# Kernel optimization log

Hardware: AMD Instinct MI355X
Metric: run time of the kernel (lower is better)

Reference implementation:

```python
import jax, jax.numpy as jnp
import numpy as np

D, W, H = 128, 128, 128          # volume obj_shape (d, w, h)
RES_SCALE = 1.4
RES_D = int(D * RES_SCALE)       # 179 detector rows
RES_H = int(H * RES_SCALE)       # 179 detector cols
N_PROJ = 10


def setup_inputs() -> dict:
    key = jax.random.key(0)
    k1, k2 = jax.random.split(key, 2)
    # learnable reconstruction volume, initialized to ones (torch.ones_like)
    I_rec = jnp.ones((1, 1, D, W, H), dtype=jnp.float32)
    # emitter positions, scaled to volume size; y-component kept away from the
    # source plane y=0 so that ray directions are well-conditioned
    poses = jax.random.uniform(k1, (50, 3), dtype=jnp.float32)
    poses = poses * jnp.array([D, W, H], jnp.float32) + jnp.array([-64.0, 256.0, -64.0], jnp.float32)
    idx = jax.random.randint(k2, (N_PROJ,), 0, 50, dtype=jnp.int32)
    return {"I_rec": I_rec, "poses": poses, "idx": idx}


def _trilinear_3d(vol, coords):
    """torch F.grid_sample 3D, bilinear, align_corners=False, zero padding.
    vol: [D, Hd, Wd]; coords: [..., 3] in (x, y, z) normalized to [-1, 1],
    where x indexes the last (Wd) axis, y the middle, z the first."""
    Dv, Hv, Wv = vol.shape
    x, y, z = coords[..., 0], coords[..., 1], coords[..., 2]
    ix = ((x + 1.0) * Wv - 1.0) * 0.5
    iy = ((y + 1.0) * Hv - 1.0) * 0.5
    iz = ((z + 1.0) * Dv - 1.0) * 0.5
    x0f, y0f, z0f = jnp.floor(ix), jnp.floor(iy), jnp.floor(iz)
    tx, ty, tz = ix - x0f, iy - y0f, iz - z0f
    x0 = x0f.astype(jnp.int32); y0 = y0f.astype(jnp.int32); z0 = z0f.astype(jnp.int32)
    x1, y1, z1 = x0 + 1, y0 + 1, z0 + 1

    def gather(zc, yc, xc):
        valid = (zc >= 0) & (zc < Dv) & (yc >= 0) & (yc < Hv) & (xc >= 0) & (xc < Wv)
        v = vol[jnp.clip(zc, 0, Dv - 1), jnp.clip(yc, 0, Hv - 1), jnp.clip(xc, 0, Wv - 1)]
        return jnp.where(valid, v, 0.0)

    out = (
        gather(z0, y0, x0) * (1 - tz) * (1 - ty) * (1 - tx)
        + gather(z0, y0, x1) * (1 - tz) * (1 - ty) * tx
        + gather(z0, y1, x0) * (1 - tz) * ty * (1 - tx)
        + gather(z0, y1, x1) * (1 - tz) * ty * tx
        + gather(z1, y0, x0) * tz * (1 - ty) * (1 - tx)
        + gather(z1, y0, x1) * tz * (1 - ty) * tx
        + gather(z1, y1, x0) * tz * ty * (1 - tx)
        + gather(z1, y1, x1) * tz * ty * tx
    )
    return out


def _project_one(vol, emi):
    """vol: [D, W, H]; emi: [3] emitter position. Returns [RES_D, RES_H]."""
    lin_x = jnp.linspace(-RES_D / 2.0, RES_D / 2.0 - 1.0, RES_D, dtype=jnp.float32)
    lin_y = jnp.linspace(-RES_H / 2.0, RES_H / 2.0 - 1.0, RES_H, dtype=jnp.float32)
    gx, gy = jnp.meshgrid(lin_x, lin_y, indexing="ij")            # [Gx, Gy]
    rays = jnp.stack([gx, jnp.zeros_like(gx), gy], axis=-1) - emi  # [Gx, Gy, 3]
    rays = rays / jnp.linalg.norm(rays, axis=-1, keepdims=True)
    dx = jnp.abs(1.0 / rays[..., 1])                               # [Gx, Gy]
    # (P0 - I0) . N  with N = (0,1,0): source-plane y samples minus emitter y
    p0y = jnp.linspace(0.0, W - 1.0, W, dtype=jnp.float32)         # [K=W]
    T = (1.0 / rays[..., 1])[..., None] * (p0y - emi[1])           # [Gx, Gy, K]
    grid = rays[..., None, :] * T[..., None] + emi                 # [Gx, Gy, K, 3]
    g0 = grid[..., 0] / D * 2.0
    g1 = grid[..., 1] / W * 2.0 - 1.0
    g2 = grid[..., 2] / H * 2.0
    coords = jnp.stack([g2, g1, g0], axis=-1)  # torch.flip(grid, [3]) -> (x,y,z)
    samp = _trilinear_3d(vol, coords)          # [Gx, Gy, K]
    return jnp.sum(samp, axis=-1) * dx


def reference(I_rec, poses, idx):
    sel = poses[idx]  # [10, 3]
    vol = I_rec[0, 0]
    projections = jax.vmap(lambda e: _project_one(vol, e))(sel)  # [10, Gx, Gy]
    return projections[None], idx
```

## Files before the change

### kernel.cpp

```cpp
#include <hip/hip_runtime.h>
#include <hip/hip_bf16.h>
#include <stdint.h>


#define DVOL   128
#define RES    179
#define NPROJ  10
#define OUT_PROJ (NPROJ * RES * RES)
#define BATCH  8

#define IL_A   132
#define IL_C   130
#define IL_SLAB (IL_C * IL_A)
#define IL_TOT  (DVOL * IL_SLAB)

__device__ __forceinline__ uint32_t bfbits(float v) {
    __hip_bfloat16 h = __float2bfloat16(v);
    return (uint32_t)*(unsigned short*)&h;
}

__global__ __launch_bounds__(128) void pad_kernel(const float* __restrict__ vol,
                                                  uint32_t* __restrict__ il) {
    const int q = blockIdx.x;
    const int p = blockIdx.y;
    const int a = threadIdx.x;
    const int wlo = q * 17;
    const int whi = min(130, wlo + 17);
    uint32_t* slab = il + p * IL_SLAB;

    uint32_t prev = 0;
    {
        const int c = wlo - 1;
        if (c >= 0 && c < 128) {
            const float* src = vol + (c << 14) + (p << 7) + a;
            float v = src[0];
            if (p >= 1) v += src[-128];
            prev = bfbits(v);
        }
    }
    #pragma unroll 2
    for (int c = wlo; c < whi; ++c) {
        uint32_t cur = 0;
        if (c < 128) {
            const float* src = vol + (c << 14) + (p << 7) + a;
            float v = src[0];
            if (p >= 1) v += src[-128];
            cur = bfbits(v);
        }
        slab[c * IL_A + (a + 1)] = (cur << 16) | prev;
        prev = cur;
    }
    for (int b = a; b < (whi - wlo) * 4; b += 128) {
        const int w  = wlo + (b >> 2);
        const int bi = b & 3;
        const int ai = (bi == 0) ? 0 : (128 + bi);
        slab[w * IL_A + ai] = 0u;
    }
}

__device__ __forceinline__ void axis_interval(float base, float slope, float lo, float hi,
                                              float& t0, float& t1) {
    if (fabsf(slope) < 1e-9f) {
        const bool in = (base >= lo && base <= hi);
        t0 = in ? -1e30f : 1e30f;
        t1 = in ?  1e30f : -1e30f;
    } else {
        const float inv = 1.0f / slope;
        const float a = (lo - base) * inv;
        const float b = (hi - base) * inv;
        t0 = fminf(a, b);
        t1 = fmaxf(a, b);
    }
}

__device__ __forceinline__ int wave_imin(int v) {
    #pragma unroll
    for (int o = 32; o; o >>= 1) v = min(v, __shfl_xor(v, o, 64));
    return v;
}
__device__ __forceinline__ int wave_imax(int v) {
    #pragma unroll
    for (int o = 32; o; o >>= 1) v = max(v, __shfl_xor(v, o, 64));
    return v;
}

__device__ __forceinline__ float asf(uint32_t u) { return __uint_as_float(u); }

__global__ __launch_bounds__(128) void proj_fast(
    const uint32_t* __restrict__ il,
    const float* __restrict__ poses,
    const int* __restrict__ idx,
    float* __restrict__ out)
{
    __shared__ uint2 tab[2][DVOL];

    const int lane = threadIdx.x & 63;
    const int wid  = threadIdx.x >> 6;
    int gj = blockIdx.x * 64 + lane;
    int gi = blockIdx.y * 2 + wid;
    const int j = blockIdx.z;

    if (blockIdx.x == 0 && blockIdx.y == 0 && j == 0 && threadIdx.x < NPROJ)
        out[OUT_PROJ + threadIdx.x] = (float)idx[threadIdx.x];

    const bool store_ok = (gi < RES) && (gj < RES);
    gi = min(gi, RES - 1);
    gj = min(gj, RES - 1);

    const int pid = idx[j];
    const float ex = poses[pid * 3 + 0];
    const float ey = poses[pid * 3 + 1];
    const float ez = poses[pid * 3 + 2];

    const float pdx = (float)gi - 89.5f;
    const float pdz = (float)gj - 89.5f;

    const float inv_ey = 1.0f / ey;
    const float sx = (ex - pdx) * inv_ey;
    const float sz = (ez - pdz) * inv_ey;
    const float ddx = pdx - ex, ddz = pdz - ez;
    const float dxw = sqrtf(ddx * ddx + ey * ey + ddz * ddz) * fabsf(inv_ey);
    const float cb = pdx + 63.5f;
    const float ab = pdz + 63.5f;

    float gc0, gc1, ga0, ga1;
    axis_interval(cb, sx, -1.0f, 128.0f, gc0, gc1);
    axis_interval(ab, sz, -1.0f, 128.0f, ga0, ga1);
    const float q_lo = fmaxf(fmaxf(gc0, ga0), 0.0f);
    const float q_hi = fminf(fminf(gc1, ga1), 127.0f);
    int q0, q1;
    if (q_lo <= q_hi + 0.5f) {
        q0 = max(0, (int)ceilf(q_lo) - 1);
        q1 = min(DVOL, (int)floorf(q_hi) + 2);
    } else { q0 = DVOL; q1 = 0; }
    int Q0 = wave_imin(q0);
    int Q1 = wave_imax(q1);
    Q0 = __builtin_amdgcn_readfirstlane(Q0);
    Q1 = __builtin_amdgcn_readfirstlane(Q1);

    const int n = Q1 - Q0;
    for (int e = lane; e < n; e += 64) {
        const int p = Q0 + e;
        const float cfc = fminf(fmaxf(fmaf((float)p, sx, cb), -1.0f), 128.0f);
        const float c0f = floorf(cfc);
        const int c0 = (int)c0f;
        uint2 t;
        t.x = __float_as_uint(cfc - c0f);
        t.y = (uint32_t)(p * IL_SLAB + (c0 + 1) * IL_A + 1);
        tab[wid][e] = t;
    }

    float acc = 0.0f;
    int pe = 0;
    float af = fmaf((float)Q0, sz, ab);

    for (; pe + (BATCH - 1) < n; pe += BATCH) {
        float tc[BATCH], ta[BATCH];
        uint2 w[BATCH];
        #pragma unroll
        for (int k = 0; k < BATCH; ++k) {
            const uint2 t = tab[wid][pe + k];
            tc[k] = asf(t.x);
            const float afc = fminf(fmaxf(fmaf((float)k, sz, af), -1.0f), 128.0f);
            const float a0f = floorf(afc);
            ta[k] = afc - a0f;
            const int a0 = (int)a0f;
            w[k] = *(const uint2*)(il + t.y + a0);
        }
        #pragma unroll
        for (int k = 0; k < BATCH; ++k) {
            const float f00 = asf(w[k].x << 16);
            const float f10 = asf(w[k].x & 0xffff0000u);
            const float f01 = asf(w[k].y << 16);
            const float f11 = asf(w[k].y & 0xffff0000u);
            const float h0 = fmaf(ta[k], f01 - f00, f00);
            const float h1 = fmaf(ta[k], f11 - f10, f10);
            acc += fmaf(tc[k], h1 - h0, h0);
        }
        af += (float)BATCH * sz;
    }
    for (; pe < n; ++pe) {
        const uint2 t = tab[wid][pe];
        const float tc = asf(t.x);
        const float afc = fminf(fmaxf(af, -1.0f), 128.0f);
        const float a0f = floorf(afc);
        const float ta = afc - a0f;
        const int a0 = (int)a0f;
        const uint2 w2 = *(const uint2*)(il + t.y + a0);
        const float f00 = asf(w2.x << 16);
        const float f10 = asf(w2.x & 0xffff0000u);
        const float f01 = asf(w2.y << 16);
        const float f11 = asf(w2.y & 0xffff0000u);
        const float h0 = fmaf(ta, f01 - f00, f00);
        const float h1 = fmaf(ta, f11 - f10, f10);
        acc += fmaf(tc, h1 - h0, h0);
        af += sz;
    }

    if (store_ok) out[j * (RES * RES) + gi * RES + gj] = acc * (0.5f * dxw);
}

__global__ __launch_bounds__(256) void proj_kernel_fb(
    const float* __restrict__ vol, const float* __restrict__ poses,
    const int* __restrict__ idx, float* __restrict__ out)
{
    const int gj = blockIdx.x * 64 + (threadIdx.x & 63);
    const int gi = blockIdx.y * 4 + (threadIdx.x >> 6);
    const int j  = blockIdx.z;
    if (blockIdx.x == 0 && blockIdx.y == 0 && j == 0 && threadIdx.x < NPROJ)
        out[OUT_PROJ + threadIdx.x] = (float)idx[threadIdx.x];
    if (gi >= RES || gj >= RES) return;
    const int pid = idx[j];
    const float ex = poses[pid*3+0], ey = poses[pid*3+1], ez = poses[pid*3+2];
    const float pdx = (float)gi - 89.5f, pdz = (float)gj - 89.5f;
    const float inv_ey = 1.0f / ey;
    const float sx = (ex - pdx) * inv_ey, sz = (ez - pdz) * inv_ey;
    const float ddx = pdx - ex, ddz = pdz - ez;
    const float dxw = sqrtf(ddx*ddx + ey*ey + ddz*ddz) * fabsf(inv_ey);
    const float cb = pdx + 63.5f, ab = pdz + 63.5f;
    float acc = 0.0f;
    for (int p = 0; p < DVOL; ++p) {
        const float cf = fmaf((float)p, sx, cb);
        const float af = fmaf((float)p, sz, ab);
        if (cf >= -1.0f && cf < 128.0f && af >= -1.0f && af < 128.0f) {
            const float c0f = floorf(cf), a0f = floorf(af);
            const float tc = cf - c0f, ta = af - a0f;
            const int c0 = (int)c0f, a0 = (int)a0f;
            const float wc0 = (c0 >= 0)   ? (1.0f - tc) : 0.0f;
            const float wc1 = (c0 <= 126) ? tc          : 0.0f;
            const float wa0 = (a0 >= 0)   ? (1.0f - ta) : 0.0f;
            const float wa1 = (a0 <= 126) ? ta          : 0.0f;
            const int c0c = c0 < 0 ? 0 : c0;
            const int c1c = c0 >= 127 ? 127 : c0 + 1;
            const int a0c = a0 < 0 ? 0 : a0;
            const int a1c = a0 >= 127 ? 127 : a0 + 1;
            const float w00 = wc0*wa0, w01 = wc0*wa1, w10 = wc1*wa0, w11 = wc1*wa1;
            const int b0 = (c0c << 14) + (p << 7);
            const int b1 = (c1c << 14) + (p << 7);
            float s = w00*vol[b0+a0c] + w01*vol[b0+a1c] + w10*vol[b1+a0c] + w11*vol[b1+a1c];
            if (p >= 1)
                s += w00*vol[b0+a0c-128] + w01*vol[b0+a1c-128]
                   + w10*vol[b1+a0c-128] + w11*vol[b1+a1c-128];
            acc += 0.5f * s;
        }
    }
    out[j * (RES * RES) + gi * RES + gj] = acc * dxw;
}

extern "C" void kernel_launch(void* const* d_in, const int* in_sizes, int n_in,
                              void* d_out, int out_size, void* d_ws, size_t ws_size,
                              hipStream_t stream) {
    const float* vol   = (const float*)d_in[0];
    const float* poses = (const float*)d_in[1];
    const int*   idx   = (const int*)d_in[2];
    float* out = (float*)d_out;

    if (ws_size >= (size_t)IL_TOT * sizeof(uint32_t)) {
        uint32_t* ilbuf = (uint32_t*)d_ws;
        dim3 pgrid(8, DVOL);
        pad_kernel<<<pgrid, 128, 0, stream>>>(vol, ilbuf);
        dim3 grid(3 , 90 , NPROJ);
        proj_fast<<<grid, 128, 0, stream>>>(ilbuf, poses, idx, out);
    } else {
        dim3 grid(3, 45, NPROJ);
        proj_kernel_fb<<<grid, 256, 0, stream>>>(vol, poses, idx, out);
    }
}
```

Before: 93.83 us.

## Double-buffer gather batches to overlap loads with interpolation math

Restructures the per-ray sampling loop into a two-buffer software pipeline: the next batch of eight bf16-pair gathers is issued before the current batch is interpolated and accumulated. This aims to hide global-memory latency behind ALU work within each wave. It also recomputes the sample coordinate from the base offset instead of accumulating it, which changes rounding slightly. In exchange it roughly doubles the live registers held for in-flight loads, which may lower occupancy.

```diff
diff --git a/kernel.cpp b/kernel.cpp
--- a/kernel.cpp
+++ b/kernel.cpp
@@ -85,6 +85,33 @@
 }
 
 __device__ __forceinline__ float asf(uint32_t u) { return __uint_as_float(u); }
+
+#define ISSUE(tc_, ta_, w_, b_) do {                                          \
+    const int base_ = (b_) * BATCH;                                           \
+    const float afb_ = fmaf((float)base_, sz, af0);                           \
+    _Pragma("unroll")                                                         \
+    for (int k = 0; k < BATCH; ++k) {                                         \
+        const uint2 t = tab[wid][base_ + k];           \
+        tc_[k] = asf(t.x);                                                    \
+        const float afc = fminf(fmaxf(fmaf((float)k, sz, afb_), -1.0f), 128.0f);\
+        const float a0f = floorf(afc);                                        \
+        ta_[k] = afc - a0f;                                                   \
+        w_[k] = *(const uint2*)(il + t.y + (int)a0f);                         \
+    }                                                                         \
+} while (0)
+
+#define CONSUME(tc_, ta_, w_) do {                                            \
+    _Pragma("unroll")                                                         \
+    for (int k = 0; k < BATCH; ++k) {                                         \
+        const float f00 = asf(w_[k].x << 16);          \
+        const float f10 = asf(w_[k].x & 0xffff0000u);  \
+        const float f01 = asf(w_[k].y << 16);          \
+        const float f11 = asf(w_[k].y & 0xffff0000u);  \
+        const float h0 = fmaf(ta_[k], f01 - f00, f00);                        \
+        const float h1 = fmaf(ta_[k], f11 - f10, f10);                        \
+        acc += fmaf(tc_[k], h1 - h0, h0);                                     \
+    }                                                                         \
+} while (0)
 
 __global__ __launch_bounds__(128) void proj_fast(
     const uint32_t* __restrict__ il,
@@ -151,42 +178,40 @@
     }
 
     float acc = 0.0f;
-    int pe = 0;
-    float af = fmaf((float)Q0, sz, ab);
-
-    for (; pe + (BATCH - 1) < n; pe += BATCH) {
-        float tc[BATCH], ta[BATCH];
-        uint2 w[BATCH];
-        #pragma unroll
-        for (int k = 0; k < BATCH; ++k) {
-            const uint2 t = tab[wid][pe + k];
-            tc[k] = asf(t.x);
-            const float afc = fminf(fmaxf(fmaf((float)k, sz, af), -1.0f), 128.0f);
-            const float a0f = floorf(afc);
-            ta[k] = afc - a0f;
-            const int a0 = (int)a0f;
-            w[k] = *(const uint2*)(il + t.y + a0);
-        }
-        #pragma unroll
-        for (int k = 0; k < BATCH; ++k) {
-            const float f00 = asf(w[k].x << 16);
-            const float f10 = asf(w[k].x & 0xffff0000u);
-            const float f01 = asf(w[k].y << 16);
-            const float f11 = asf(w[k].y & 0xffff0000u);
-            const float h0 = fmaf(ta[k], f01 - f00, f00);
-            const float h1 = fmaf(ta[k], f11 - f10, f10);
-            acc += fmaf(tc[k], h1 - h0, h0);
-        }
-        af += (float)BATCH * sz;
-    }
-    for (; pe < n; ++pe) {
+    const float af0 = fmaf((float)Q0, sz, ab);
+
+    float tcA[BATCH], taA[BATCH]; uint2 wA[BATCH];
+    float tcB[BATCH], taB[BATCH]; uint2 wB[BATCH];
+
+    const int nb = (n > 0) ? (n >> 3) : 0;
+    if (nb >= 2) {
+        ISSUE(tcA, taA, wA, 0);
+        int b = 0;
+        for (; b + 2 < nb; b += 2) {
+            ISSUE(tcB, taB, wB, b + 1);
+            CONSUME(tcA, taA, wA);
+            ISSUE(tcA, taA, wA, b + 2);
+            CONSUME(tcB, taB, wB);
+        }
+        if (b + 1 < nb) {
+            ISSUE(tcB, taB, wB, b + 1);
+            CONSUME(tcA, taA, wA);
+            CONSUME(tcB, taB, wB);
+        } else {
+            CONSUME(tcA, taA, wA);
+        }
+    } else if (nb == 1) {
+        ISSUE(tcA, taA, wA, 0);
+        CONSUME(tcA, taA, wA);
+    }
+
+    for (int pe = nb << 3; pe < n; ++pe) {
         const uint2 t = tab[wid][pe];
         const float tc = asf(t.x);
-        const float afc = fminf(fmaxf(af, -1.0f), 128.0f);
+        const float afc = fminf(fmaxf(fmaf((float)pe, sz, af0), -1.0f), 128.0f);
         const float a0f = floorf(afc);
         const float ta = afc - a0f;
-        const int a0 = (int)a0f;
-        const uint2 w2 = *(const uint2*)(il + t.y + a0);
+        const uint2 w2 = *(const uint2*)(il + t.y + (int)a0f);
         const float f00 = asf(w2.x << 16);
         const float f10 = asf(w2.x & 0xffff0000u);
         const float f01 = asf(w2.y << 16);
@@ -194,7 +219,6 @@
         const float h0 = fmaf(ta, f01 - f00, f00);
         const float h1 = fmaf(ta, f11 - f10, f10);
         acc += fmaf(tc, h1 - h0, h0);
-        af += sz;
     }
 
     if (store_ok) out[j * (RES * RES) + gi * RES + gj] = acc * (0.5f * dxw);
```

Result: no change. 92.49 us (-1.4%).
